# Optimization experiments

Hardware: AMD Instinct MI355X
Metric: run time of the kernel (lower is better)

The kernel has to match this reference:

```python
import jax, jax.numpy as jnp
import numpy as np

BS, DOP, RAN, AZI, ELE = 2, 32, 128, 128, 32
INTERVAL = 0.1
TAU = 1.0


def setup_inputs() -> dict:
    key = jax.random.key(0)
    ks = jax.random.split(key, 7)
    N = RAN * AZI * ELE
    seg = jax.random.normal(ks[0], (BS, N, 1), jnp.float32)
    flow = jax.random.normal(ks[1], (BS, N, 3), jnp.float32) * 2.0
    x1 = jax.random.normal(ks[2], (BS, DOP, RAN, AZI, ELE), jnp.float32)
    dop_arr = jax.random.normal(ks[3], (BS, DOP), jnp.float32)
    coords = jax.random.uniform(ks[4], (BS, 3, RAN, AZI, ELE), jnp.float32)
    ori = jax.random.normal(ks[5], (BS, 3, RAN, AZI, ELE), jnp.float32)
    u = jax.random.uniform(ks[6], (BS, DOP, RAN, AZI, ELE), jnp.float32,
                           minval=1e-6, maxval=1.0 - 1e-6)
    gumbels = -jnp.log(-jnp.log(u))  # Gumbel(0,1) noise (sampled internally in torch)
    return {"seg": seg, "flow": flow, "x1": x1, "dop_arr": dop_arr,
            "coords": coords, "ori": ori, "gumbels": gumbels}


def _gather3d(vol_flat, z, y, x, H, W):
    # vol_flat: (B, C, D*H*W); z,y,x: (B, D, H, W) int32
    B = vol_flat.shape[0]
    idx = ((z * H + y) * W + x).reshape(B, 1, -1)
    g = jnp.take_along_axis(vol_flat, idx, axis=2)
    return g  # (B, C, N)


def _grid_sample_3d_border(vol, gx, gy, gz):
    # Trilinear grid_sample, padding_mode='border', align_corners=True.
    # vol: (B, C, D, H, W); gx/gy/gz: (B, D, H, W) normalized coords in [-1, 1]
    B, C, D, H, W = vol.shape
    ix = jnp.clip((gx + 1.0) * 0.5 * (W - 1), 0.0, W - 1.0)
    iy = jnp.clip((gy + 1.0) * 0.5 * (H - 1), 0.0, H - 1.0)
    iz = jnp.clip((gz + 1.0) * 0.5 * (D - 1), 0.0, D - 1.0)
    x0f, y0f, z0f = jnp.floor(ix), jnp.floor(iy), jnp.floor(iz)
    wx, wy, wz = ix - x0f, iy - y0f, iz - z0f
    x0 = jnp.clip(x0f.astype(jnp.int32), 0, W - 1)
    y0 = jnp.clip(y0f.astype(jnp.int32), 0, H - 1)
    z0 = jnp.clip(z0f.astype(jnp.int32), 0, D - 1)
    x1 = jnp.clip(x0 + 1, 0, W - 1)
    y1 = jnp.clip(y0 + 1, 0, H - 1)
    z1 = jnp.clip(z0 + 1, 0, D - 1)
    vf = vol.reshape(B, C, -1)
    out = jnp.zeros((B, C, D * H * W), vol.dtype)
    for zc, wzc in ((z0, 1.0 - wz), (z1, wz)):
        for yc, wyc in ((y0, 1.0 - wy), (y1, wy)):
            for xc, wxc in ((x0, 1.0 - wx), (x1, wx)):
                w = (wzc * wyc * wxc).reshape(B, 1, -1)
                out = out + w * _gather3d(vf, zc, yc, xc, H, W)
    return out.reshape(B, C, D, H, W)


def _warp_flowxyz(coords, flo):
    B, C, D, H, W = coords.shape
    zz = jnp.arange(D, dtype=jnp.float32)[:, None, None]
    yy = jnp.arange(H, dtype=jnp.float32)[None, :, None]
    xx = jnp.arange(W, dtype=jnp.float32)[None, None, :]
    # vgrid = base grid + flow, per channel (x, y, z)
    vx = xx + flo[:, 0]
    vy = yy + flo[:, 1]
    vz = zz + flo[:, 2]
    gx = 2.0 * vx / (W - 1) - 1.0
    gy = 2.0 * vy / (H - 1) - 1.0
    gz = 2.0 * vz / (D - 1) - 1.0
    r, a, e = coords[:, 0], coords[:, 1], coords[:, 2]
    ce = jnp.cos(e)
    xyz = jnp.stack([r * ce * jnp.cos(a), r * ce * jnp.sin(a), r * jnp.sin(e)], axis=1)
    xyz_new = _grid_sample_3d_border(xyz, gx, gy, gz)
    return xyz_new - xyz


def reference(seg, flow, x1, dop_arr, coords, ori, gumbels):
    bs, dop, ran, azi, ele = x1.shape
    dop_b = dop_arr.reshape(bs, dop, 1, 1, 1)
    # gumbel_softmax(hard=True): forward value is the hard one-hot
    y_soft = jax.nn.softmax((x1 + gumbels) / TAU, axis=1)
    idx = jnp.argmax(y_soft, axis=1)
    y_hard = jax.nn.one_hot(idx, dop, axis=1, dtype=x1.dtype)
    max_x1 = y_hard + y_soft - jax.lax.stop_gradient(y_soft)  # straight-through
    softmax_x1 = jax.nn.softmax(x1, axis=1)
    x1_dop1 = jnp.sum(max_x1 * dop_b, axis=1, keepdims=True)
    x1_dop2 = jnp.sum(softmax_x1 * dop_b, axis=1, keepdims=True)
    x1_dop = jnp.concatenate([x1_dop1, x1_dop2], axis=1)  # (bs, 2, R, A, E)
    seg_v = jnp.transpose(seg, (0, 2, 1)).reshape(bs, -1, ran, azi, ele)
    flow_v = jnp.transpose(flow, (0, 2, 1)).reshape(bs, -1, ran, azi, ele)
    flow_xyz = _warp_flowxyz(coords, flow_v)
    velo = flow_xyz / INTERVAL
    dop_label = jnp.sum(velo * ori, axis=1, keepdims=True)
    dop_error = (dop_label - x1_dop) ** 2
    seg_label = jax.nn.sigmoid(10.0 * (0.15 - dop_error))
    seg_label = jnp.mean(seg_label, axis=1, keepdims=True)
    seg_sig = jax.nn.sigmoid(seg_v)
    loss = jnp.mean(jnp.abs(seg_sig - seg_label))
    return loss
```

## Files before the change

kernel.cpp:

```cpp
#include <hip/hip_runtime.h>
#include <math.h>

#define BSZ  2
#define DOPN 32
#define RAN  128
#define AZI  128
#define ELE  32
#define NVOX (RAN * AZI * ELE)
#define TPB  256
#define VPT  2
#define DH   8

__device__ __forceinline__ float sigmoidf_(float t) {
    return 1.0f / (1.0f + __expf(-t));
}

__global__ __launch_bounds__(TPB) void xyz_precompute(
    const float* __restrict__ coords, float4* __restrict__ xyz4,
    float* __restrict__ out, int out_elems)
{
    if (blockIdx.x == 0 && blockIdx.y == 0) {
        for (int i = threadIdx.x; i < out_elems; i += TPB) out[i] = 0.0f;
    }
    const int n0 = (blockIdx.x * TPB + threadIdx.x) * 4;
    const int b = blockIdx.y;
    const float* cb = coords + (size_t)b * 3 * NVOX;
    const float4 r4 = *(const float4*)(cb + n0);
    const float4 a4 = *(const float4*)(cb + NVOX + n0);
    const float4 e4 = *(const float4*)(cb + 2 * NVOX + n0);
    const float rr[4] = { r4.x, r4.y, r4.z, r4.w };
    const float aa[4] = { a4.x, a4.y, a4.z, a4.w };
    const float ee[4] = { e4.x, e4.y, e4.z, e4.w };
    float4* op = xyz4 + (size_t)b * NVOX + n0;
    #pragma unroll
    for (int v = 0; v < 4; ++v) {
        float sa, ca, se, ce;
        __sincosf(aa[v], &sa, &ca);
        __sincosf(ee[v], &se, &ce);
        op[v] = make_float4(rr[v] * ce * ca, rr[v] * ce * sa, rr[v] * se, 0.0f);
    }
}

__global__ __launch_bounds__(TPB) void seg_dop_loss(
    const float* __restrict__ seg, const float* __restrict__ flow,
    const float* __restrict__ x1, const float* __restrict__ dop_arr,
    const float* __restrict__ ori, const float* __restrict__ gumbels,
    const float4* __restrict__ xyz4, float* __restrict__ out)
{
    __shared__ float s_dop[DOPN];
    __shared__ float s_wave[TPB / 64];

    const int b = blockIdx.y;
    if (threadIdx.x < DOPN) s_dop[threadIdx.x] = dop_arr[b * DOPN + threadIdx.x];
    __syncthreads();

    const int n0 = (blockIdx.x * TPB + threadIdx.x) * VPT;

    float m_lg[VPT] = { -3.4e38f, -3.4e38f };
    float mdop[VPT] = { 0.f, 0.f };
    float ssum[VPT] = { 0.f, 0.f };
    float wsum[VPT] = { 0.f, 0.f };

    const int par = threadIdx.x & 1;
    const int cg  = n0 & ~3;
    const float* swp = par ? gumbels : x1;
    const size_t sbase = (size_t)b * DOPN * NVOX + (size_t)cg;

    float4 q[DH];
    for (int h = 0; h < DOPN / DH; ++h) {
        #pragma unroll
        for (int d = 0; d < DH; ++d)
            q[d] = *(const float4*)(swp + sbase + (size_t)(h * DH + d) * NVOX);
        #pragma unroll
        for (int d = 0; d < DH; ++d) {
            const float dv = s_dop[h * DH + d];
            const float t0 = par ? q[d].x : q[d].z;
            const float t1 = par ? q[d].y : q[d].w;
            const float r0 = __shfl_xor(t0, 1, 64);
            const float r1 = __shfl_xor(t1, 1, 64);
            const float xv[VPT] = { par ? r0 : q[d].x, par ? r1 : q[d].y };
            const float gv[VPT] = { par ? q[d].z : r0, par ? q[d].w : r1 };
            #pragma unroll
            for (int v = 0; v < VPT; ++v) {
                const float lg = xv[v] + gv[v];
                if (lg > m_lg[v]) { m_lg[v] = lg; mdop[v] = dv; }
                const float ev = __expf(xv[v]);
                ssum[v] += ev;
                wsum[v] += ev * dv;
            }
        }
    }

    const float* fl = flow + ((size_t)b * NVOX + (size_t)n0) * 3;
    float fbuf[3 * VPT];
    *(float2*)(fbuf)     = *(const float2*)(fl);
    *(float2*)(fbuf + 2) = *(const float2*)(fl + 2);
    *(float2*)(fbuf + 4) = *(const float2*)(fl + 4);

    const float4* xb4 = xyz4 + (size_t)b * NVOX;
    float4 bxyz[VPT];
    #pragma unroll
    for (int v = 0; v < VPT; ++v) bxyz[v] = xb4[n0 + v];

    const float* ob = ori + (size_t)b * 3 * NVOX;
    const float2 oX2 = *(const float2*)(ob + n0);
    const float2 oY2 = *(const float2*)(ob + NVOX + n0);
    const float2 oZ2 = *(const float2*)(ob + 2 * NVOX + n0);
    const float oX[VPT] = { oX2.x, oX2.y };
    const float oY[VPT] = { oY2.x, oY2.y };
    const float oZ[VPT] = { oZ2.x, oZ2.y };

    const float2 sg2 = *(const float2*)(seg + (size_t)b * NVOX + n0);
    const float sg[VPT] = { sg2.x, sg2.y };

    const int xB = n0 & (ELE - 1);
    const int yI = (n0 >> 5) & (AZI - 1);
    const int zI = n0 >> 12;

    float contrib = 0.0f;
    #pragma unroll
    for (int v = 0; v < VPT; ++v) {
        const float vx = (float)(xB + v) + fbuf[3 * v + 0];
        const float vy = (float)yI       + fbuf[3 * v + 1];
        const float vz = (float)zI       + fbuf[3 * v + 2];

        const float gx = 2.0f * vx / (float)(ELE - 1) - 1.0f;
        const float gy = 2.0f * vy / (float)(AZI - 1) - 1.0f;
        const float gz = 2.0f * vz / (float)(RAN - 1) - 1.0f;
        const float ix = fminf(fmaxf((gx + 1.0f) * 0.5f * (float)(ELE - 1), 0.0f), (float)(ELE - 1));
        const float iy = fminf(fmaxf((gy + 1.0f) * 0.5f * (float)(AZI - 1), 0.0f), (float)(AZI - 1));
        const float iz = fminf(fmaxf((gz + 1.0f) * 0.5f * (float)(RAN - 1), 0.0f), (float)(RAN - 1));

        const float x0f = floorf(ix), y0f = floorf(iy), z0f = floorf(iz);
        const float wx = ix - x0f, wy = iy - y0f, wz = iz - z0f;
        int x0 = (int)x0f; x0 = x0 < 0 ? 0 : (x0 > ELE - 1 ? ELE - 1 : x0);
        int y0 = (int)y0f; y0 = y0 < 0 ? 0 : (y0 > AZI - 1 ? AZI - 1 : y0);
        int z0 = (int)z0f; z0 = z0 < 0 ? 0 : (z0 > RAN - 1 ? RAN - 1 : z0);
        const int x1c = x0 + 1 > ELE - 1 ? ELE - 1 : x0 + 1;
        const int y1c = y0 + 1 > AZI - 1 ? AZI - 1 : y0 + 1;
        const int z1c = z0 + 1 > RAN - 1 ? RAN - 1 : z0 + 1;

        const int m00 = (z0  * AZI + y0 ) * ELE;
        const int m01 = (z0  * AZI + y1c) * ELE;
        const int m10 = (z1c * AZI + y0 ) * ELE;
        const int m11 = (z1c * AZI + y1c) * ELE;
        const float4 c000 = xb4[m00 + x0],  c001 = xb4[m00 + x1c];
        const float4 c010 = xb4[m01 + x0],  c011 = xb4[m01 + x1c];
        const float4 c100 = xb4[m10 + x0],  c101 = xb4[m10 + x1c];
        const float4 c110 = xb4[m11 + x0],  c111 = xb4[m11 + x1c];

        const float w000 = (1.0f - wz) * (1.0f - wy) * (1.0f - wx);
        const float w001 = (1.0f - wz) * (1.0f - wy) * wx;
        const float w010 = (1.0f - wz) * wy * (1.0f - wx);
        const float w011 = (1.0f - wz) * wy * wx;
        const float w100 = wz * (1.0f - wy) * (1.0f - wx);
        const float w101 = wz * (1.0f - wy) * wx;
        const float w110 = wz * wy * (1.0f - wx);
        const float w111 = wz * wy * wx;

        const float sX = w000*c000.x + w001*c001.x + w010*c010.x + w011*c011.x
                       + w100*c100.x + w101*c101.x + w110*c110.x + w111*c111.x;
        const float sY = w000*c000.y + w001*c001.y + w010*c010.y + w011*c011.y
                       + w100*c100.y + w101*c101.y + w110*c110.y + w111*c111.y;
        const float sZ = w000*c000.z + w001*c001.z + w010*c010.z + w011*c011.z
                       + w100*c100.z + w101*c101.z + w110*c110.z + w111*c111.z;

        const float vX = (sX - bxyz[v].x) * 10.0f;
        const float vY = (sY - bxyz[v].y) * 10.0f;
        const float vZ = (sZ - bxyz[v].z) * 10.0f;
        const float dop_label = vX * oX[v] + vY * oY[v] + vZ * oZ[v];

        const float dop1 = mdop[v];
        const float dop2 = wsum[v] / ssum[v];
        float e1 = dop_label - dop1; e1 *= e1;
        float e2 = dop_label - dop2; e2 *= e2;
        const float seg_label = 0.5f * (sigmoidf_(10.0f * (0.15f - e1)) +
                                        sigmoidf_(10.0f * (0.15f - e2)));
        contrib += fabsf(sigmoidf_(sg[v]) - seg_label);
    }

    #pragma unroll
    for (int off = 32; off > 0; off >>= 1)
        contrib += __shfl_down(contrib, off, 64);
    const int lane = threadIdx.x & 63;
    const int wid  = threadIdx.x >> 6;
    if (lane == 0) s_wave[wid] = contrib;
    __syncthreads();
    if (threadIdx.x == 0) {
        float bsum = 0.0f;
        #pragma unroll
        for (int w = 0; w < TPB / 64; ++w) bsum += s_wave[w];
        atomicAdd(out, bsum * (1.0f / ((float)BSZ * (float)NVOX)));
    }
}

extern "C" void kernel_launch(void* const* d_in, const int* in_sizes, int n_in,
                              void* d_out, int out_size, void* d_ws, size_t ws_size,
                              hipStream_t stream) {
    const float* seg    = (const float*)d_in[0];
    const float* flow   = (const float*)d_in[1];
    const float* x1     = (const float*)d_in[2];
    const float* dopar  = (const float*)d_in[3];
    const float* coords = (const float*)d_in[4];
    const float* ori    = (const float*)d_in[5];
    const float* gumb   = (const float*)d_in[6];
    float* out = (float*)d_out;
    float4* xyz4 = (float4*)d_ws;

    dim3 gridA(NVOX / (TPB * 4), BSZ);
    xyz_precompute<<<gridA, TPB, 0, stream>>>(coords, xyz4, out, out_size);
    dim3 gridB(NVOX / (TPB * VPT), BSZ);
    seg_dop_loss<<<gridB, TPB, 0, stream>>>(seg, flow, x1, dopar, ori, gumb, xyz4, out);
}
```

Baseline: 324.5 us.

## Split doppler channel sweep into separate kernel, writing per-voxel dop pair to workspace

Moves the 32-channel gumbel-argmax and softmax-weighted doppler reduction out of the loss kernel into a dedicated dop_sweep kernel. That kernel writes the two doppler values per voxel to workspace, and the loss kernel reads them back alongside the trilinear gather. The sweep now loads x1 and gumbels directly as float2, dropping the lane-pair shuffle, and uses 16 channels per batch of loads. The goal is a streaming-bandwidth kernel and a lighter gather kernel, each with better occupancy. The cost is an extra launch and an additional 16 bytes per voxel written and read back.

Measured after the change: 345.7 us. +6.5%, slower.

```diff
diff --git a/kernel.cpp b/kernel.cpp
--- a/kernel.cpp
+++ b/kernel.cpp
@@ -9,10 +9,58 @@
 #define NVOX (RAN * AZI * ELE)
 #define TPB  256
 #define VPT  2
-#define DH   8
+#define DH   16
 
 __device__ __forceinline__ float sigmoidf_(float t) {
     return 1.0f / (1.0f + __expf(-t));
+}
+
+__global__ __launch_bounds__(TPB) void dop_sweep(
+    const float* __restrict__ x1, const float* __restrict__ gumbels,
+    const float* __restrict__ dop_arr, float2* __restrict__ dop12)
+{
+    __shared__ float s_dop[DOPN];
+    const int b = blockIdx.y;
+    if (threadIdx.x < DOPN) s_dop[threadIdx.x] = dop_arr[b * DOPN + threadIdx.x];
+    __syncthreads();
+
+    const int n0 = (blockIdx.x * TPB + threadIdx.x) * VPT;
+    const size_t base = (size_t)b * DOPN * NVOX + (size_t)n0;
+
+    float m_lg[VPT] = { -3.4e38f, -3.4e38f };
+    float mdop[VPT] = { 0.f, 0.f };
+    float ssum[VPT] = { 0.f, 0.f };
+    float wsum[VPT] = { 0.f, 0.f };
+
+    for (int h = 0; h < 2; ++h) {
+        const size_t dbase = base + (size_t)h * DH * NVOX;
+        float2 xa[DH], ga[DH];
+        #pragma unroll
+        for (int d = 0; d < DH; ++d)
+            xa[d] = *(const float2*)(x1 + dbase + (size_t)d * NVOX);
+        #pragma unroll
+        for (int d = 0; d < DH; ++d)
+            ga[d] = *(const float2*)(gumbels + dbase + (size_t)d * NVOX);
+        #pragma unroll
+        for (int d = 0; d < DH; ++d) {
+            const float dv = s_dop[h * DH + d];
+            const float xv[VPT] = { xa[d].x, xa[d].y };
+            const float gv[VPT] = { ga[d].x, ga[d].y };
+            #pragma unroll
+            for (int v = 0; v < VPT; ++v) {
+                const float lg = xv[v] + gv[v];
+                if (lg > m_lg[v]) { m_lg[v] = lg; mdop[v] = dv; }
+                const float ev = __expf(xv[v]);
+                ssum[v] += ev;
+                wsum[v] += ev * dv;
+            }
+        }
+    }
+
+    float4 st;
+    st.x = mdop[0]; st.y = wsum[0] / ssum[0];
+    st.z = mdop[1]; st.w = wsum[1] / ssum[1];
+    *(float4*)(dop12 + (size_t)b * NVOX + n0) = st;
 }
 
 __global__ __launch_bounds__(TPB) void xyz_precompute(
@@ -41,55 +89,19 @@
     }
 }
 
-__global__ __launch_bounds__(TPB) void seg_dop_loss(
+__global__ __launch_bounds__(TPB) void seg_gather_loss(
     const float* __restrict__ seg, const float* __restrict__ flow,
-    const float* __restrict__ x1, const float* __restrict__ dop_arr,
-    const float* __restrict__ ori, const float* __restrict__ gumbels,
+    const float* __restrict__ ori, const float2* __restrict__ dop12,
     const float4* __restrict__ xyz4, float* __restrict__ out)
 {
-    __shared__ float s_dop[DOPN];
     __shared__ float s_wave[TPB / 64];
 
     const int b = blockIdx.y;
-    if (threadIdx.x < DOPN) s_dop[threadIdx.x] = dop_arr[b * DOPN + threadIdx.x];
-    __syncthreads();
-
     const int n0 = (blockIdx.x * TPB + threadIdx.x) * VPT;
 
-    float m_lg[VPT] = { -3.4e38f, -3.4e38f };
-    float mdop[VPT] = { 0.f, 0.f };
-    float ssum[VPT] = { 0.f, 0.f };
-    float wsum[VPT] = { 0.f, 0.f };
-
-    const int par = threadIdx.x & 1;
-    const int cg  = n0 & ~3;
-    const float* swp = par ? gumbels : x1;
-    const size_t sbase = (size_t)b * DOPN * NVOX + (size_t)cg;
-
-    float4 q[DH];
-    for (int h = 0; h < DOPN / DH; ++h) {
-        #pragma unroll
-        for (int d = 0; d < DH; ++d)
-            q[d] = *(const float4*)(swp + sbase + (size_t)(h * DH + d) * NVOX);
-        #pragma unroll
-        for (int d = 0; d < DH; ++d) {
-            const float dv = s_dop[h * DH + d];
-            const float t0 = par ? q[d].x : q[d].z;
-            const float t1 = par ? q[d].y : q[d].w;
-            const float r0 = __shfl_xor(t0, 1, 64);
-            const float r1 = __shfl_xor(t1, 1, 64);
-            const float xv[VPT] = { par ? r0 : q[d].x, par ? r1 : q[d].y };
-            const float gv[VPT] = { par ? q[d].z : r0, par ? q[d].w : r1 };
-            #pragma unroll
-            for (int v = 0; v < VPT; ++v) {
-                const float lg = xv[v] + gv[v];
-                if (lg > m_lg[v]) { m_lg[v] = lg; mdop[v] = dv; }
-                const float ev = __expf(xv[v]);
-                ssum[v] += ev;
-                wsum[v] += ev * dv;
-            }
-        }
-    }
+    const float4 dp = *(const float4*)(dop12 + (size_t)b * NVOX + n0);
+    const float dop1v[VPT] = { dp.x, dp.z };
+    const float dop2v[VPT] = { dp.y, dp.w };
 
     const float* fl = flow + ((size_t)b * NVOX + (size_t)n0) * 3;
     float fbuf[3 * VPT];
@@ -170,10 +182,8 @@
         const float vZ = (sZ - bxyz[v].z) * 10.0f;
         const float dop_label = vX * oX[v] + vY * oY[v] + vZ * oZ[v];
 
-        const float dop1 = mdop[v];
-        const float dop2 = wsum[v] / ssum[v];
-        float e1 = dop_label - dop1; e1 *= e1;
-        float e2 = dop_label - dop2; e2 *= e2;
+        float e1 = dop_label - dop1v[v]; e1 *= e1;
+        float e2 = dop_label - dop2v[v]; e2 *= e2;
         const float seg_label = 0.5f * (sigmoidf_(10.0f * (0.15f - e1)) +
                                         sigmoidf_(10.0f * (0.15f - e2)));
         contrib += fabsf(sigmoidf_(sg[v]) - seg_label);
@@ -205,10 +215,16 @@
     const float* ori    = (const float*)d_in[5];
     const float* gumb   = (const float*)d_in[6];
     float* out = (float*)d_out;
-    float4* xyz4 = (float4*)d_ws;
+
+    float4* xyz4  = (float4*)d_ws;
+    float2* dop12 = (float2*)((char*)d_ws + (size_t)BSZ * NVOX * sizeof(float4));
+
+    dim3 gridS(NVOX / (TPB * VPT), BSZ);
+    dop_sweep<<<gridS, TPB, 0, stream>>>(x1, gumb, dopar, dop12);
 
     dim3 gridA(NVOX / (TPB * 4), BSZ);
     xyz_precompute<<<gridA, TPB, 0, stream>>>(coords, xyz4, out, out_size);
-    dim3 gridB(NVOX / (TPB * VPT), BSZ);
-    seg_dop_loss<<<gridB, TPB, 0, stream>>>(seg, flow, x1, dopar, ori, gumb, xyz4, out);
-}
+
+    dim3 gridG(NVOX / (TPB * VPT), BSZ);
+    seg_gather_loss<<<gridG, TPB, 0, stream>>>(seg, flow, ori, dop12, xyz4, out);
+}
```
